# Kernel tuning notes

Hardware: AMD Instinct MI355X
Metric: run time of the kernel (lower is better)

Reference implementation:

```python
import jax, jax.numpy as jnp
import numpy as np

B, L, E = 2, 8192, 1024
H, D = 16, 64          # num_heads, head_dim
W, G = 512, 64         # window_size, group_size


def _rope(x):
    # x: [B, H, S, D]. Faithful to original (with the obvious pe-indexing fix):
    # pe[:,0::2]=sin(pos*inv_freq), pe[:,1::2]=cos(pos*inv_freq)
    S, Dh = x.shape[-2], x.shape[-1]
    pos = jnp.arange(S, dtype=jnp.float32)[:, None]                     # [S,1]
    inv_freq = 1.0 / (10000.0 ** (jnp.arange(0, Dh, 2, dtype=jnp.float32) / Dh))
    ang = pos * inv_freq                                                # [S, D/2]
    sin, cos = jnp.sin(ang), jnp.cos(ang)
    xe, xo = x[..., 0::2], x[..., 1::2]
    # cat(even_rotated, odd_rotated) along last dim, as in original
    return jnp.concatenate([xe * sin + xo * cos, -xe * cos + xo * sin], axis=-1)


def setup_inputs() -> dict:
    key = jax.random.key(0)
    ks = jax.random.split(key, 11)
    s = 0.02  # keep pre-softmax logits well-scaled
    return {
        "query": jax.random.normal(ks[0], (B, L, E), jnp.float32),
        "key":   jax.random.normal(ks[1], (B, L, E), jnp.float32),
        "value": jax.random.normal(ks[2], (B, L, E), jnp.float32),
        "Wq": jax.random.normal(ks[3], (E, E), jnp.float32) * s,
        "bq": jax.random.normal(ks[4], (E,), jnp.float32) * s,
        "Wk": jax.random.normal(ks[5], (E, E), jnp.float32) * s,
        "bk": jax.random.normal(ks[6], (E,), jnp.float32) * s,
        "Wv": jax.random.normal(ks[7], (E, E), jnp.float32) * s,
        "bv": jax.random.normal(ks[8], (E,), jnp.float32) * s,
        "Wo": jax.random.normal(ks[9], (E, E), jnp.float32) * s,
        "bo": jax.random.normal(ks[10], (E,), jnp.float32) * s,
    }


def reference(query, key, value, Wq, bq, Wk, bk, Wv, bv, Wo, bo):
    Bq, Lq, _ = query.shape
    Lk = key.shape[1]
    # projections (torch Linear: x @ W.T + b), split heads -> [B, H, L, D]
    def proj(x, Wt, b):
        y = x @ Wt.T + b
        return y.reshape(Bq, -1, H, D).transpose(0, 2, 1, 3)
    q = _rope(proj(query, Wq, bq))
    k = _rope(proj(key, Wk, bk))
    v = proj(value, Wv, bv)

    # sliding-window grouped scores: for each group starting at idx=n*G,
    # score against keys[idx : min(idx+W, Lk)], zero-fill the tail.
    n_groups = Lq // G
    starts = jnp.arange(n_groups) * G                                    # [N]
    kidx = starts[:, None] + jnp.arange(W)[None, :]                      # [N, W]
    valid = kidx < Lk                                                    # [N, W]
    kidx_c = jnp.minimum(kidx, Lk - 1)
    k_blk = k[:, :, kidx_c]                                              # [B,H,N,W,D]
    q_grp = q.reshape(Bq, H, n_groups, G, D)                             # [B,H,N,G,D]
    scores = jnp.einsum('bhngd,bhnwd->bhngw', q_grp, k_blk) / (D ** 0.5)
    scores = jnp.where(valid[None, None, :, None, :], scores, 0.0)       # zero-fill tail
    scores = scores.reshape(Bq, H, Lq, W)                                # [B,H,Lq,W]

    probs = jax.nn.softmax(scores, axis=-1)                              # softmax over W incl. zeros (faithful)
    ctx = jnp.einsum('bhqw,bhwd->bhqd', probs, v[:, :, :W])              # faithful: first-W values only
    ctx = ctx.transpose(0, 2, 1, 3).reshape(Bq, Lq, H * D)
    return ctx @ Wo.T + bo
```

## Files before the change

### kernel.cpp

```cpp
#include <hip/hip_runtime.h>


typedef unsigned short ushort_t;
typedef __attribute__((ext_vector_type(8))) __bf16 bf16x8;
typedef __attribute__((ext_vector_type(4))) float f32x4;
typedef __attribute__((ext_vector_type(8))) unsigned short ushort8;
typedef __attribute__((ext_vector_type(4))) unsigned int u32x4;

#define MFMA16(a, b, c) __builtin_amdgcn_mfma_f32_16x16x32_bf16((a), (b), (c), 0, 0, 0)

static __device__ __forceinline__ ushort_t f2bf(float f) {
    unsigned u = __float_as_uint(f);
    u += 0x7fffu + ((u >> 16) & 1u);
    return (ushort_t)(u >> 16);
}

static __device__ __forceinline__ ushort_t f2bfc(float f) {
    __bf16 h = (__bf16)f;
    return __builtin_bit_cast(ushort_t, h);
}

typedef __attribute__((address_space(3))) unsigned int lds_u32;
typedef const __attribute__((address_space(1))) unsigned int glb_u32;

static __device__ __forceinline__ void gload_lds16(const void* g, void* l) {
    __builtin_amdgcn_global_load_lds((glb_u32*)g, (lds_u32*)l, 16, 0, 0);
}

__global__ __launch_bounds__(256) void cvt_bf16(const float* __restrict__ in,
                                                ushort_t* __restrict__ out, long n8) {
    long i = (long)blockIdx.x * 256 + threadIdx.x;
    if (i >= n8) return;
    const float4* p = (const float4*)in + i * 2;
    float4 a = p[0], b = p[1];
    ushort8 o;
    o[0] = f2bf(a.x); o[1] = f2bf(a.y); o[2] = f2bf(a.z); o[3] = f2bf(a.w);
    o[4] = f2bf(b.x); o[5] = f2bf(b.y); o[6] = f2bf(b.z); o[7] = f2bf(b.w);
    *(ushort8*)(out + i * 8) = o;
}

__global__ __launch_bounds__(256) void cvt_value(const float* __restrict__ in,
                                                 ushort_t* __restrict__ out) {
    int i = blockIdx.x * 256 + threadIdx.x;
    int f = i * 8;
    int m = f >> 10, c = f & 1023;
    long src = ((long)(m >> 9) * 8192 + (m & 511)) * 1024 + c;
    const float4* p = (const float4*)(in + src);
    float4 a = p[0], b = p[1];
    ushort8 o;
    o[0] = f2bf(a.x); o[1] = f2bf(a.y); o[2] = f2bf(a.z); o[3] = f2bf(a.w);
    o[4] = f2bf(b.x); o[5] = f2bf(b.y); o[6] = f2bf(b.z); o[7] = f2bf(b.w);
    *(ushort8*)(out + f) = o;
}

__global__ __launch_bounds__(256) void rope_tab(float2* __restrict__ tab) {
    int i = blockIdx.x * 256 + threadIdx.x;
    int l = i >> 5, j = i & 31;
    float inv = exp2f(-(float)j * 0.4152410118609203f);
    float a = (float)l * inv;
    tab[i] = make_float2(sinf(a), cosf(a));
}

template <int MODE>
__global__ __launch_bounds__(256) void gemm_bt(const ushort_t* __restrict__ A,
                                               const ushort_t* __restrict__ Bw,
                                               const float* __restrict__ bias,
                                               void* __restrict__ outp,
                                               const float2* __restrict__ rope) {
    __shared__ __align__(16) ushort_t sA[128 * 32];
    __shared__ __align__(16) ushort_t sB[128 * 32];
    const int tid = threadIdx.x, lane = tid & 63, wv = tid >> 6;
    const int wr = wv >> 1, wc = wv & 1;
    const long bm = (long)blockIdx.x * 128;
    const int bn = blockIdx.y * 128;

    f32x4 acc[4][4] = {};

    const int srow = tid >> 2;
    const int sslot = tid & 3;
    const int ca = sslot ^ (srow & 3);
    const ushort_t* Ab = A + (bm + srow) * 1024 + ca * 8;
    const ushort_t* Bb = Bw + (long)(bn + srow) * 1024 + ca * 8;
    ushort_t* la = &sA[srow * 32 + sslot * 8];
    ushort_t* lb = &sB[srow * 32 + sslot * 8];

    for (int kt = 0; kt < 32; ++kt) {
        const int ko = kt * 32;
        gload_lds16(Ab + ko, la);
        gload_lds16(Ab + 64 * 1024 + ko, la + 64 * 32);
        gload_lds16(Bb + ko, lb);
        gload_lds16(Bb + 64 * 1024 + ko, lb + 64 * 32);
        __syncthreads();
        bf16x8 af[4], bfr[4];
#pragma unroll
        for (int mt = 0; mt < 4; ++mt) {
            int r = wr * 64 + mt * 16 + (lane & 15);
            int sl = (lane >> 4) ^ (r & 3);
            af[mt] = *(const bf16x8*)&sA[r * 32 + sl * 8];
        }
#pragma unroll
        for (int nt = 0; nt < 4; ++nt) {
            int r = wc * 64 + nt * 16 + (lane & 15);
            int sl = (lane >> 4) ^ (r & 3);
            bfr[nt] = *(const bf16x8*)&sB[r * 32 + sl * 8];
        }
#pragma unroll
        for (int mt = 0; mt < 4; ++mt)
#pragma unroll
            for (int nt = 0; nt < 4; ++nt)
                acc[mt][nt] = MFMA16(af[mt], bfr[nt], acc[mt][nt]);
        __syncthreads();
    }

    if constexpr (MODE == 2) {
        float* out = (float*)outp;
#pragma unroll
        for (int nt = 0; nt < 4; ++nt) {
            int col = bn + wc * 64 + nt * 16 + (lane & 15);
            float bs = bias[col];
#pragma unroll
            for (int mt = 0; mt < 4; ++mt) {
                long g0 = bm + wr * 64 + mt * 16 + ((lane >> 4) << 2);
#pragma unroll
                for (int r = 0; r < 4; ++r)
                    out[(g0 + r) * 1024 + col] = acc[mt][nt][r] + bs;
            }
        }
    } else if constexpr (MODE == 1) {
        __shared__ __align__(16) ushort_t sE[4][4096];
        ushort_t* out = (ushort_t*)outp;
        ushort_t* se = &sE[wv][0];
#pragma unroll
        for (int nt = 0; nt < 4; ++nt) {
            int col = bn + wc * 64 + nt * 16 + (lane & 15);
            float bs = bias[col];
            int c = (col & 63) >> 1;
            int outd = ((col & 1) ? 32 : 0) + c;
            int chunk = outd >> 3, dlo = outd & 7;
#pragma unroll
            for (int mt = 0; mt < 4; ++mt) {
#pragma unroll
                for (int r = 0; r < 4; ++r) {
                    float y = acc[mt][nt][r] + bs;
                    float yp = __shfl_xor(y, 1);
                    int row = mt * 16 + ((lane >> 4) << 2) + r;
                    int l = ((int)bm + wr * 64 + row) & 8191;
                    float2 sc = rope[l * 32 + c];
                    float val = (col & 1) ? (y * sc.x - yp * sc.y)
                                          : (y * sc.x + yp * sc.y);
                    se[row * 64 + ((chunk ^ (row & 7)) << 3) + dlo] = f2bf(val);
                }
            }
        }
        asm volatile("s_waitcnt lgkmcnt(0)" ::: "memory");
        int hh = (bn + wc * 64) >> 6;
#pragma unroll
        for (int i = 0; i < 8; ++i) {
            int row = i * 8 + (lane >> 3);
            int cb = lane & 7;
            ushort8 vv = *(const ushort8*)&se[row * 64 + ((cb ^ (row & 7)) << 3)];
            int m = (int)bm + wr * 64 + row;
            int bb = m >> 13, l = m & 8191;
            *(ushort8*)&out[(((long)(bb * 16 + hh)) * 8192 + l) * 64 + cb * 8] = vv;
        }
    } else {
        ushort_t* out = (ushort_t*)outp;
#pragma unroll
        for (int nt = 0; nt < 4; ++nt) {
            int col = bn + wc * 64 + nt * 16 + (lane & 15);
            float bs = bias[col];
            int hh = col >> 6, d = col & 63;
#pragma unroll
            for (int mt = 0; mt < 4; ++mt) {
                int m0 = (int)bm + wr * 64 + mt * 16 + ((lane >> 4) << 2);
#pragma unroll
                for (int r = 0; r < 4; ++r) {
                    int m = m0 + r;
                    int bb = m >> 9, w = m & 511;
                    int t = w & 31;
                    int s = (t < 16) ? ((t >> 2) * 8 + (t & 3))
                                     : (((t & 15) >> 2) * 8 + 4 + (t & 3));
                    int wp = (w & ~31) | s;
                    out[(((long)(bb * 16 + hh)) * 64 + d) * 512 + wp] =
                        f2bf(acc[mt][nt][r] + bs);
                }
            }
        }
    }
}

__global__ __launch_bounds__(256) void attn(const ushort_t* __restrict__ qr,
                                            const ushort_t* __restrict__ kr,
                                            const ushort_t* __restrict__ vT,
                                            ushort_t* __restrict__ ctx) {
    __shared__ __align__(16) ushort_t sK[512 * 64];
    __shared__ __align__(16) ushort_t sE[4][1024];
    const int bid = blockIdx.x;
    const int gc = bid & 15, h = (bid >> 4) & 15, b = bid >> 8;
    const int tid = threadIdx.x, lane = tid & 63, wv = tid >> 6;

    const f32x4 kZero = {0.f, 0.f, 0.f, 0.f};
    const u32x4 kOneU = {0x3F803F80u, 0x3F803F80u, 0x3F803F80u, 0x3F803F80u};
    const bf16x8 vone = __builtin_bit_cast(bf16x8, kOneU);

    const ushort_t* khead = kr + ((long)(b * 16 + h)) * 8192 * 64;
    const ushort_t* qhead = qr + ((long)(b * 16 + h)) * 8192 * 64;
    const ushort_t* vb = vT + ((long)(b * 16 + h)) * 64 * 512;

    {
        const long base = (long)gc * 512;
#pragma unroll
        for (int i = 0; i < 16; ++i) {
            int idx = i * 256 + tid;
            int row = idx >> 3, sl = idx & 7;
            int chunk = sl ^ (row & 7);
            gload_lds16(khead + (base + row) * 64 + chunk * 8,
                        (char*)sK + idx * 16);
        }
    }
    __syncthreads();

    ushort_t* se = &sE[wv][0];

#pragma unroll 1
    for (int gi = 0; gi < 8; ++gi) {
        const int g = gc * 8 + gi;
        const int start = g * 64;
        const int climit = 8192 - start;
        const bool anymask = (climit < 512);

        const int qrow = start + wv * 16 + (lane & 15);
        const ushort_t* qp = qhead + (long)qrow * 64 + ((lane >> 4) * 8);
        bf16x8 aq0 = *(const bf16x8*)qp;
        bf16x8 aq1 = *(const bf16x8*)(qp + 32);

        f32x4 o[4];
#pragma unroll
        for (int d0 = 0; d0 < 4; ++d0) o[d0] = kZero;
        f32x4 o4 = kZero;

#pragma unroll
        for (int kc = 0; kc < 16; ++kc) {
            if (kc == 2) {
                __syncthreads();
                if (gi < 7) {
#pragma unroll
                    for (int i = 0; i < 2; ++i) {
                        int idx = i * 256 + tid;
                        int rrel = idx >> 3, sl = idx & 7;
                        long rg = (long)start + 512 + rrel;
                        int chunk = sl ^ ((int)rg & 7);
                        long rc = rg > 8191 ? 8191 : rg;
                        gload_lds16(khead + rc * 64 + chunk * 8,
                                    (char*)sK + (start & 511) * 128 + idx * 16);
                    }
                }
            }
            int c0 = kc * 32 + (lane & 15);
            int c1 = c0 + 16;
            int slot0 = (start + c0) & 511, x0 = slot0 & 7;
            int slot1 = (start + c1) & 511, x1 = slot1 & 7;
            bf16x8 kb00 = *(const bf16x8*)&sK[slot0 * 64 + (((lane >> 4)) ^ x0) * 8];
            bf16x8 kb01 = *(const bf16x8*)&sK[slot0 * 64 + ((4 + (lane >> 4)) ^ x0) * 8];
            bf16x8 kb10 = *(const bf16x8*)&sK[slot1 * 64 + (((lane >> 4)) ^ x1) * 8];
            bf16x8 kb11 = *(const bf16x8*)&sK[slot1 * 64 + ((4 + (lane >> 4)) ^ x1) * 8];
            f32x4 s0 = MFMA16(kb00, aq0, kZero);
            s0 = MFMA16(kb01, aq1, s0);
            f32x4 s1 = MFMA16(kb10, aq0, kZero);
            s1 = MFMA16(kb11, aq1, s1);

            const int k0 = kc * 32 + ((lane >> 4) << 2);
            float p0[4], p1[4];
#pragma unroll
            for (int r = 0; r < 4; ++r) {
                p0[r] = exp2f(s0[r] * 0.18033688011112042f);
                p1[r] = exp2f(s1[r] * 0.18033688011112042f);
            }
            if (anymask) {
#pragma unroll
                for (int r = 0; r < 4; ++r) {
                    if (k0 + r >= climit) p0[r] = 1.0f;
                    if (k0 + 16 + r >= climit) p1[r] = 1.0f;
                }
            }
            bf16x8 pa;
            pa[0] = (__bf16)p0[0]; pa[1] = (__bf16)p0[1];
            pa[2] = (__bf16)p0[2]; pa[3] = (__bf16)p0[3];
            pa[4] = (__bf16)p1[0]; pa[5] = (__bf16)p1[1];
            pa[6] = (__bf16)p1[2]; pa[7] = (__bf16)p1[3];

#pragma unroll
            for (int d0 = 0; d0 < 4; ++d0) {
                bf16x8 bvf = *(const bf16x8*)&vb[(long)(d0 * 16 + (lane & 15)) * 512 +
                                                 kc * 32 + (lane >> 4) * 8];
                o[d0] = MFMA16(pa, bvf, o[d0]);
            }
            o4 = MFMA16(pa, vone, o4);
        }

        float si[4];
#pragma unroll
        for (int r = 0; r < 4; ++r) si[r] = __builtin_amdgcn_rcpf(o4[r]);

#pragma unroll
        for (int d0 = 0; d0 < 4; ++d0) {
#pragma unroll
            for (int r = 0; r < 4; ++r) {
                int row = ((lane >> 4) << 2) + r;
                int d = d0 * 16 + (lane & 15);
                se[row * 64 + (((d >> 3) ^ (row & 7)) << 3) + (d & 7)] =
                    f2bfc(o[d0][r] * si[r]);
            }
        }
        asm volatile("s_waitcnt lgkmcnt(0)" ::: "memory");
#pragma unroll
        for (int i = 0; i < 2; ++i) {
            int row = i * 8 + (lane >> 3);
            int cb = lane & 7;
            ushort8 vv = *(const ushort8*)&se[row * 64 + ((cb ^ (row & 7)) << 3)];
            int l = start + wv * 16 + row;
            *(ushort8*)&ctx[((long)(b * 8192 + l)) * 1024 + h * 64 + cb * 8] = vv;
        }
    }
}

extern "C" void kernel_launch(void* const* d_in, const int* in_sizes, int n_in,
                              void* d_out, int out_size, void* d_ws, size_t ws_size,
                              hipStream_t stream) {
    const float* query = (const float*)d_in[0];
    const float* key_ = (const float*)d_in[1];
    const float* value = (const float*)d_in[2];
    const float* Wq = (const float*)d_in[3];
    const float* bq = (const float*)d_in[4];
    const float* Wk = (const float*)d_in[5];
    const float* bk = (const float*)d_in[6];
    const float* Wv = (const float*)d_in[7];
    const float* bv = (const float*)d_in[8];
    const float* Wo = (const float*)d_in[9];
    const float* bo = (const float*)d_in[10];
    float* out = (float*)d_out;
    char* ws = (char*)d_ws;

    ushort_t* Xbf = (ushort_t*)(ws);
    ushort_t* Wqb = (ushort_t*)(ws + 33554432L);
    ushort_t* Wkb = (ushort_t*)(ws + 33554432L + 2097152L);
    ushort_t* Wvb = (ushort_t*)(ws + 33554432L + 2 * 2097152L);
    ushort_t* Wob = (ushort_t*)(ws + 33554432L + 3 * 2097152L);
    float2* rope = (float2*)(ws + 41943040L);
    ushort_t* qrb = (ushort_t*)(ws + 44040192L);
    ushort_t* krb = (ushort_t*)(ws + 77594624L);
    ushort_t* vin = (ushort_t*)(ws + 111149056L);
    ushort_t* vTb = (ushort_t*)(ws + 113246208L);

    rope_tab<<<1024, 256, 0, stream>>>(rope);
    cvt_bf16<<<512, 256, 0, stream>>>(Wq, Wqb, 131072);
    cvt_bf16<<<512, 256, 0, stream>>>(Wk, Wkb, 131072);
    cvt_bf16<<<512, 256, 0, stream>>>(Wv, Wvb, 131072);
    cvt_bf16<<<512, 256, 0, stream>>>(Wo, Wob, 131072);

    cvt_bf16<<<8192, 256, 0, stream>>>(query, Xbf, 2097152);
    gemm_bt<1><<<dim3(128, 8), 256, 0, stream>>>(Xbf, Wqb, bq, qrb, rope);
    cvt_bf16<<<8192, 256, 0, stream>>>(key_, Xbf, 2097152);
    gemm_bt<1><<<dim3(128, 8), 256, 0, stream>>>(Xbf, Wkb, bk, krb, rope);
    cvt_value<<<512, 256, 0, stream>>>(value, vin);
    gemm_bt<3><<<dim3(8, 8), 256, 0, stream>>>(vin, Wvb, bv, vTb, nullptr);

    attn<<<512, 256, 0, stream>>>(qrb, krb, vTb, Xbf);
    gemm_bt<2><<<dim3(128, 8), 256, 0, stream>>>(Xbf, Wob, bo, out, nullptr);
}
```

Before: 358.9 us.

## Software-pipeline attention QK and PV, fold softmax scale into Q, drop ones-MFMA

Restructures the attention inner loop so the QK^T MFMAs and exp for the next key chunk are issued alongside the PV MFMAs of the current chunk, giving latency overlap. The softmax scale (1/sqrt(D)·log2e) moves into the Q projection epilogue, removing a multiply per score. The row-sum ones-vector MFMA is replaced by a scalar accumulation plus cross-lane shuffles. LDS addressing is also precomputed with XOR offsets. The change raises register pressure, and the row sum is now taken over fp32 probabilities rather than bf16-rounded ones.

```diff
diff --git a/kernel.cpp b/kernel.cpp
--- a/kernel.cpp
+++ b/kernel.cpp
@@ -5,7 +5,6 @@
 typedef __attribute__((ext_vector_type(8))) __bf16 bf16x8;
 typedef __attribute__((ext_vector_type(4))) float f32x4;
 typedef __attribute__((ext_vector_type(8))) unsigned short ushort8;
-typedef __attribute__((ext_vector_type(4))) unsigned int u32x4;
 
 #define MFMA16(a, b, c) __builtin_amdgcn_mfma_f32_16x16x32_bf16((a), (b), (c), 0, 0, 0)
 
@@ -66,7 +65,8 @@
                                                const ushort_t* __restrict__ Bw,
                                                const float* __restrict__ bias,
                                                void* __restrict__ outp,
-                                               const float2* __restrict__ rope) {
+                                               const float2* __restrict__ rope,
+                                               float oscale) {
     __shared__ __align__(16) ushort_t sA[128 * 32];
     __shared__ __align__(16) ushort_t sB[128 * 32];
     const int tid = threadIdx.x, lane = tid & 63, wv = tid >> 6;
@@ -146,8 +146,8 @@
                     int row = mt * 16 + ((lane >> 4) << 2) + r;
                     int l = ((int)bm + wr * 64 + row) & 8191;
                     float2 sc = rope[l * 32 + c];
-                    float val = (col & 1) ? (y * sc.x - yp * sc.y)
-                                          : (y * sc.x + yp * sc.y);
+                    float val = ((col & 1) ? (y * sc.x - yp * sc.y)
+                                           : (y * sc.x + yp * sc.y)) * oscale;
                     se[row * 64 + ((chunk ^ (row & 7)) << 3) + dlo] = f2bf(val);
                 }
             }
@@ -200,12 +200,18 @@
     const int tid = threadIdx.x, lane = tid & 63, wv = tid >> 6;
 
     const f32x4 kZero = {0.f, 0.f, 0.f, 0.f};
-    const u32x4 kOneU = {0x3F803F80u, 0x3F803F80u, 0x3F803F80u, 0x3F803F80u};
-    const bf16x8 vone = __builtin_bit_cast(bf16x8, kOneU);
 
     const ushort_t* khead = kr + ((long)(b * 16 + h)) * 8192 * 64;
     const ushort_t* qhead = qr + ((long)(b * 16 + h)) * 8192 * 64;
     const ushort_t* vb = vT + ((long)(b * 16 + h)) * 64 * 512;
+
+    const int xc0 = (((lane >> 4) ^ (lane & 7)) << 4);
+    const int xc1 = ((((lane >> 4) + 4) ^ (lane & 7)) << 4);
+    const ushort_t* vbl = vb + (lane & 15) * 512 + ((lane >> 4) << 3);
+    const ushort_t* vp0 = vbl;
+    const ushort_t* vp1 = vbl + 8192;
+    const ushort_t* vp2 = vbl + 16384;
+    const ushort_t* vp3 = vbl + 24576;
 
     {
         const long base = (long)gc * 512;
@@ -221,6 +227,7 @@
     __syncthreads();
 
     ushort_t* se = &sE[wv][0];
+    const char* skc = (const char*)sK;
 
 #pragma unroll 1
     for (int gi = 0; gi < 8; ++gi) {
@@ -234,10 +241,46 @@
         bf16x8 aq0 = *(const bf16x8*)qp;
         bf16x8 aq1 = *(const bf16x8*)(qp + 32);
 
+        const int rowbase = ((start + (lane & 15)) * 128) & 65535;
+
         f32x4 o[4];
 #pragma unroll
         for (int d0 = 0; d0 < 4; ++d0) o[d0] = kZero;
-        f32x4 o4 = kZero;
+        float ssum = 0.f;
+        bf16x8 pa;
+
+        {
+            int rb = rowbase;
+            int rb1 = (rb + 2048) & 65535;
+            bf16x8 kb00 = *(const bf16x8*)(skc + (rb | xc0));
+            bf16x8 kb01 = *(const bf16x8*)(skc + (rb | xc1));
+            bf16x8 kb10 = *(const bf16x8*)(skc + (rb1 | xc0));
+            bf16x8 kb11 = *(const bf16x8*)(skc + (rb1 | xc1));
+            f32x4 s0 = MFMA16(kb00, aq0, kZero);
+            s0 = MFMA16(kb01, aq1, s0);
+            f32x4 s1 = MFMA16(kb10, aq0, kZero);
+            s1 = MFMA16(kb11, aq1, s1);
+            float p0[4], p1[4];
+#pragma unroll
+            for (int r = 0; r < 4; ++r) {
+                p0[r] = exp2f(s0[r]);
+                p1[r] = exp2f(s1[r]);
+            }
+            if (anymask) {
+                const int k0 = ((lane >> 4) << 2);
+#pragma unroll
+                for (int r = 0; r < 4; ++r) {
+                    if (k0 + r >= climit) p0[r] = 1.0f;
+                    if (k0 + 16 + r >= climit) p1[r] = 1.0f;
+                }
+            }
+#pragma unroll
+            for (int r = 0; r < 4; ++r) ssum += p0[r] + p1[r];
+            pa[0] = (__bf16)p0[0]; pa[1] = (__bf16)p0[1];
+            pa[2] = (__bf16)p0[2]; pa[3] = (__bf16)p0[3];
+            pa[4] = (__bf16)p1[0]; pa[5] = (__bf16)p1[1];
+            pa[6] = (__bf16)p1[2]; pa[7] = (__bf16)p1[3];
+        }
 
 #pragma unroll
         for (int kc = 0; kc < 16; ++kc) {
@@ -256,51 +299,54 @@
                     }
                 }
             }
-            int c0 = kc * 32 + (lane & 15);
-            int c1 = c0 + 16;
-            int slot0 = (start + c0) & 511, x0 = slot0 & 7;
-            int slot1 = (start + c1) & 511, x1 = slot1 & 7;
-            bf16x8 kb00 = *(const bf16x8*)&sK[slot0 * 64 + (((lane >> 4)) ^ x0) * 8];
-            bf16x8 kb01 = *(const bf16x8*)&sK[slot0 * 64 + ((4 + (lane >> 4)) ^ x0) * 8];
-            bf16x8 kb10 = *(const bf16x8*)&sK[slot1 * 64 + (((lane >> 4)) ^ x1) * 8];
-            bf16x8 kb11 = *(const bf16x8*)&sK[slot1 * 64 + ((4 + (lane >> 4)) ^ x1) * 8];
-            f32x4 s0 = MFMA16(kb00, aq0, kZero);
-            s0 = MFMA16(kb01, aq1, s0);
-            f32x4 s1 = MFMA16(kb10, aq0, kZero);
-            s1 = MFMA16(kb11, aq1, s1);
-
-            const int k0 = kc * 32 + ((lane >> 4) << 2);
-            float p0[4], p1[4];
-#pragma unroll
-            for (int r = 0; r < 4; ++r) {
-                p0[r] = exp2f(s0[r] * 0.18033688011112042f);
-                p1[r] = exp2f(s1[r] * 0.18033688011112042f);
-            }
-            if (anymask) {
+            f32x4 s0 = kZero, s1 = kZero;
+            if (kc < 15) {
+                int rb = (rowbase + (kc + 1) * 4096) & 65535;
+                int rb1 = (rb + 2048) & 65535;
+                bf16x8 kb00 = *(const bf16x8*)(skc + (rb | xc0));
+                bf16x8 kb01 = *(const bf16x8*)(skc + (rb | xc1));
+                bf16x8 kb10 = *(const bf16x8*)(skc + (rb1 | xc0));
+                bf16x8 kb11 = *(const bf16x8*)(skc + (rb1 | xc1));
+                s0 = MFMA16(kb00, aq0, kZero);
+                s0 = MFMA16(kb01, aq1, s0);
+                s1 = MFMA16(kb10, aq0, kZero);
+                s1 = MFMA16(kb11, aq1, s1);
+            }
+            o[0] = MFMA16(pa, *(const bf16x8*)(vp0 + kc * 32), o[0]);
+            o[1] = MFMA16(pa, *(const bf16x8*)(vp1 + kc * 32), o[1]);
+            o[2] = MFMA16(pa, *(const bf16x8*)(vp2 + kc * 32), o[2]);
+            o[3] = MFMA16(pa, *(const bf16x8*)(vp3 + kc * 32), o[3]);
+            if (kc < 15) {
+                float p0[4], p1[4];
 #pragma unroll
                 for (int r = 0; r < 4; ++r) {
-                    if (k0 + r >= climit) p0[r] = 1.0f;
-                    if (k0 + 16 + r >= climit) p1[r] = 1.0f;
-                }
-            }
-            bf16x8 pa;
-            pa[0] = (__bf16)p0[0]; pa[1] = (__bf16)p0[1];
-            pa[2] = (__bf16)p0[2]; pa[3] = (__bf16)p0[3];
-            pa[4] = (__bf16)p1[0]; pa[5] = (__bf16)p1[1];
-            pa[6] = (__bf16)p1[2]; pa[7] = (__bf16)p1[3];
-
-#pragma unroll
-            for (int d0 = 0; d0 < 4; ++d0) {
-                bf16x8 bvf = *(const bf16x8*)&vb[(long)(d0 * 16 + (lane & 15)) * 512 +
-                                                 kc * 32 + (lane >> 4) * 8];
-                o[d0] = MFMA16(pa, bvf, o[d0]);
-            }
-            o4 = MFMA16(pa, vone, o4);
-        }
-
+                    p0[r] = exp2f(s0[r]);
+                    p1[r] = exp2f(s1[r]);
+                }
+                if (anymask) {
+                    const int k0 = (kc + 1) * 32 + ((lane >> 4) << 2);
+#pragma unroll
+                    for (int r = 0; r < 4; ++r) {
+                        if (k0 + r >= climit) p0[r] = 1.0f;
+                        if (k0 + 16 + r >= climit) p1[r] = 1.0f;
+                    }
+                }
+#pragma unroll
+                for (int r = 0; r < 4; ++r) ssum += p0[r] + p1[r];
+                pa[0] = (__bf16)p0[0]; pa[1] = (__bf16)p0[1];
+                pa[2] = (__bf16)p0[2]; pa[3] = (__bf16)p0[3];
+                pa[4] = (__bf16)p1[0]; pa[5] = (__bf16)p1[1];
+                pa[6] = (__bf16)p1[2]; pa[7] = (__bf16)p1[3];
+            }
+        }
+
+        ssum += __shfl_xor(ssum, 16);
+        ssum += __shfl_xor(ssum, 32);
+        float rin = __builtin_amdgcn_rcpf(ssum);
         float si[4];
 #pragma unroll
-        for (int r = 0; r < 4; ++r) si[r] = __builtin_amdgcn_rcpf(o4[r]);
+        for (int r = 0; r < 4; ++r)
+            si[r] = __shfl(rin, ((lane >> 4) << 2) + r);
 
 #pragma unroll
         for (int d0 = 0; d0 < 4; ++d0) {
@@ -352,6 +398,8 @@
     ushort_t* vin = (ushort_t*)(ws + 111149056L);
     ushort_t* vTb = (ushort_t*)(ws + 113246208L);
 
+    const float kQScale = 0.18033688011112042f;
+
     rope_tab<<<1024, 256, 0, stream>>>(rope);
     cvt_bf16<<<512, 256, 0, stream>>>(Wq, Wqb, 131072);
     cvt_bf16<<<512, 256, 0, stream>>>(Wk, Wkb, 131072);
@@ -359,12 +407,12 @@
     cvt_bf16<<<512, 256, 0, stream>>>(Wo, Wob, 131072);
 
     cvt_bf16<<<8192, 256, 0, stream>>>(query, Xbf, 2097152);
-    gemm_bt<1><<<dim3(128, 8), 256, 0, stream>>>(Xbf, Wqb, bq, qrb, rope);
+    gemm_bt<1><<<dim3(128, 8), 256, 0, stream>>>(Xbf, Wqb, bq, qrb, rope, kQScale);
     cvt_bf16<<<8192, 256, 0, stream>>>(key_, Xbf, 2097152);
-    gemm_bt<1><<<dim3(128, 8), 256, 0, stream>>>(Xbf, Wkb, bk, krb, rope);
+    gemm_bt<1><<<dim3(128, 8), 256, 0, stream>>>(Xbf, Wkb, bk, krb, rope, 1.0f);
     cvt_value<<<512, 256, 0, stream>>>(value, vin);
-    gemm_bt<3><<<dim3(8, 8), 256, 0, stream>>>(vin, Wvb, bv, vTb, nullptr);
+    gemm_bt<3><<<dim3(8, 8), 256, 0, stream>>>(vin, Wvb, bv, vTb, nullptr, 1.0f);
 
     attn<<<512, 256, 0, stream>>>(qrb, krb, vTb, Xbf);
-    gemm_bt<2><<<dim3(128, 8), 256, 0, stream>>>(Xbf, Wob, bo, out, nullptr);
-}
+    gemm_bt<2><<<dim3(128, 8), 256, 0, stream>>>(Xbf, Wob, bo, out, nullptr, 1.0f);
+}
```

New measurement: 470.0 us. 30.9% more time.
